# Optimization experiments

Hardware: AMD Instinct MI355X
Metric: run time of the kernel (lower is better)

Reference implementation:

```python
import jax, jax.numpy as jnp
import numpy as np

D_K, D_V, H, N = 128, 256, 256, 50
B, L = 128, 1024

def setup_inputs() -> dict:
    key = jax.random.key(0)
    ks = jax.random.split(key, 10)
    s = lambda fan_in: 1.0 / np.sqrt(fan_in)
    return {
        'problems': jax.random.normal(ks[0], (B, L, D_K), dtype=jnp.float32),
        'interactions': jax.random.normal(ks[1], (B, L, D_V), dtype=jnp.float32),
        'w_key': jax.random.uniform(ks[2], (N, D_K), jnp.float32, -s(D_K), s(D_K)),
        'w_erase_w': jax.random.uniform(ks[3], (D_V, D_V), jnp.float32, -s(D_V), s(D_V)),
        'w_erase_b': jax.random.uniform(ks[4], (D_V,), jnp.float32, -s(D_V), s(D_V)),
        'w_add_w': jax.random.uniform(ks[5], (D_V, D_V), jnp.float32, -s(D_V), s(D_V)),
        'w_add_b': jax.random.uniform(ks[6], (D_V,), jnp.float32, -s(D_V), s(D_V)),
        'w_out_w': jax.random.uniform(ks[7], (H, D_V + D_K), jnp.float32, -s(D_V + D_K), s(D_V + D_K)),
        'w_out_b': jax.random.uniform(ks[8], (H,), jnp.float32, -s(D_V + D_K), s(D_V + D_K)),
        'init_memory': jax.random.normal(ks[9], (N, D_V), dtype=jnp.float32),
    }

def reference(problems, interactions, w_key, w_erase_w, w_erase_b, w_add_w, w_add_b, w_out_w, w_out_b, init_memory):
    # Precompute per-step gates outside the scan (they do not depend on memory)
    e = jax.nn.sigmoid(jnp.einsum('bld,ed->ble', interactions, w_erase_w) + w_erase_b)  # (B,L,d_v)
    a = jnp.tanh(jnp.einsum('bld,ed->ble', interactions, w_add_w) + w_add_b)            # (B,L,d_v)
    score = jax.nn.softmax(jnp.einsum('bld,nd->bln', problems, w_key), axis=-1)          # (B,L,n)

    mem0 = jnp.broadcast_to(init_memory, (problems.shape[0], N, D_V))

    def step(memory, xs):
        sc_t, e_t, a_t = xs  # (B,n), (B,d_v), (B,d_v)
        read = jnp.einsum('bn,bnd->bd', sc_t, memory)  # weighted read
        memory = memory * (1.0 - sc_t[:, :, None] * e_t[:, None, :])
        memory = memory + sc_t[:, :, None] * a_t[:, None, :]
        return memory, read

    xs = (score.transpose(1, 0, 2), e.transpose(1, 0, 2), a.transpose(1, 0, 2))  # time-major
    _, reads = jax.lax.scan(step, mem0, xs)  # reads: (L,B,d_v)

    x = jnp.concatenate([reads.transpose(1, 0, 2), problems], axis=-1)  # (B,L,d_v+d_k)
    # dropout in eval mode = identity
    return jnp.tanh(jnp.einsum('blc,hc->blh', x, w_out_w) + w_out_b)
```

## Files before the change

### kernel.cpp

```cpp
#include <hip/hip_runtime.h>

#define B_    128
#define L_    1024
#define DK_   128
#define DV_   256
#define NS_   50
#define H_    256
#define M_    (B_ * L_)

typedef __attribute__((ext_vector_type(8))) short   short8;
typedef __attribute__((ext_vector_type(4))) float   float4v;
typedef __attribute__((ext_vector_type(4))) int     int4v;

__device__ __forceinline__ float b2f(unsigned short u) {
    unsigned int x = ((unsigned int)u) << 16;
    return __builtin_bit_cast(float, x);
}
__device__ __forceinline__ unsigned short f2b(float f) {
    unsigned int x = __builtin_bit_cast(unsigned int, f);
    x += 0x7fffu + ((x >> 16) & 1u);
    return (unsigned short)(x >> 16);
}
__device__ __forceinline__ int pack2(float lo, float hi) {
    return (int)f2b(lo) | ((int)f2b(hi) << 16);
}
__device__ __forceinline__ float sigmoid_f(float x) {
    return 1.f / (1.f + __expf(-x));
}
__device__ __forceinline__ float tanh_f(float x) {
    return 1.f - 2.f / (__expf(2.f * x) + 1.f);
}

__device__ __forceinline__ void gload_lds16(const void* g, void* l) {
    __builtin_amdgcn_global_load_lds(
        (const __attribute__((address_space(1))) void*)g,
        (__attribute__((address_space(3))) void*)l, 16, 0, 0);
}

__global__ __launch_bounds__(256) void gate_kernel(
    const float* __restrict__ X,
    const float* __restrict__ We, const float* __restrict__ be,
    const float* __restrict__ Wa, const float* __restrict__ ba,
    unsigned short* __restrict__ e_out, unsigned short* __restrict__ a_out)
{
    constexpr int K = DV_;
    const int mblk = blockIdx.x, nblk = blockIdx.y, gate = blockIdx.z;
    const float* W    = gate ? Wa : We;
    const float* bias = gate ? ba : be;
    unsigned short* out = gate ? a_out : e_out;

    __shared__ unsigned short As[128 * 40];
    __shared__ unsigned short Bs[128 * 40];

    const int tid  = threadIdx.x;
    const int lane = tid & 63, wid = tid >> 6;
    const int wm = wid >> 1, wn = wid & 1;
    const int l15 = lane & 15, quad = lane >> 4;

    float4v acc[4][4];
#pragma unroll
    for (int i = 0; i < 4; i++)
#pragma unroll
        for (int j = 0; j < 4; j++) {
            acc[i][j][0] = 0.f; acc[i][j][1] = 0.f;
            acc[i][j][2] = 0.f; acc[i][j][3] = 0.f;
        }

    const int srow = tid >> 1;
    const int scol = (tid & 1) * 16;
    const size_t Abase = ((size_t)mblk * 128 + srow) * K;
    const size_t Bbase = ((size_t)nblk * 128 + srow) * K;

    for (int k0 = 0; k0 < K; k0 += 32) {
        const float* xa = &X[Abase + k0 + scol];
        const float* xb = &W[Bbase + k0 + scol];
        float4v va0 = *(const float4v*)(xa);
        float4v va1 = *(const float4v*)(xa + 4);
        float4v va2 = *(const float4v*)(xa + 8);
        float4v va3 = *(const float4v*)(xa + 12);
        float4v vb0 = *(const float4v*)(xb);
        float4v vb1 = *(const float4v*)(xb + 4);
        float4v vb2 = *(const float4v*)(xb + 8);
        float4v vb3 = *(const float4v*)(xb + 12);
        int4v pa0, pa1, pb0, pb1;
        pa0[0] = pack2(va0[0], va0[1]); pa0[1] = pack2(va0[2], va0[3]);
        pa0[2] = pack2(va1[0], va1[1]); pa0[3] = pack2(va1[2], va1[3]);
        pa1[0] = pack2(va2[0], va2[1]); pa1[1] = pack2(va2[2], va2[3]);
        pa1[2] = pack2(va3[0], va3[1]); pa1[3] = pack2(va3[2], va3[3]);
        pb0[0] = pack2(vb0[0], vb0[1]); pb0[1] = pack2(vb0[2], vb0[3]);
        pb0[2] = pack2(vb1[0], vb1[1]); pb0[3] = pack2(vb1[2], vb1[3]);
        pb1[0] = pack2(vb2[0], vb2[1]); pb1[1] = pack2(vb2[2], vb2[3]);
        pb1[2] = pack2(vb3[0], vb3[1]); pb1[3] = pack2(vb3[2], vb3[3]);
        *(int4v*)&As[srow * 40 + scol]     = pa0;
        *(int4v*)&As[srow * 40 + scol + 8] = pa1;
        *(int4v*)&Bs[srow * 40 + scol]     = pb0;
        *(int4v*)&Bs[srow * 40 + scol + 8] = pb1;
        __syncthreads();
        short8 af[4], bf[4];
#pragma unroll
        for (int i = 0; i < 4; i++)
            af[i] = *(const short8*)&As[(64 * wm + 16 * i + l15) * 40 + quad * 8];
#pragma unroll
        for (int j = 0; j < 4; j++)
            bf[j] = *(const short8*)&Bs[(64 * wn + 16 * j + l15) * 40 + quad * 8];
#pragma unroll
        for (int i = 0; i < 4; i++)
#pragma unroll
            for (int j = 0; j < 4; j++)
                acc[i][j] = __builtin_amdgcn_mfma_f32_16x16x32_bf16(af[i], bf[j], acc[i][j], 0, 0, 0);
        __syncthreads();
    }

#pragma unroll
    for (int i = 0; i < 4; i++) {
        const int row = mblk * 128 + 64 * wm + 16 * i + quad * 4;
#pragma unroll
        for (int j = 0; j < 4; j++) {
            const int col = nblk * 128 + 64 * wn + 16 * j + l15;
            const float bv = bias[col];
#pragma unroll
            for (int r = 0; r < 4; r++) {
                float v = acc[i][j][r] + bv;
                v = gate ? tanh_f(v) : sigmoid_f(v);
                out[(size_t)(row + r) * DV_ + col] = f2b(v);
            }
        }
    }
}

__global__ __launch_bounds__(256) void score_kernel(
    const float* __restrict__ problems,
    const float* __restrict__ w_key,
    float* __restrict__ score_scan)
{
    const int rowi = blockIdx.x * 256 + threadIdx.x;
    const float* p = problems + (size_t)rowi * DK_;

    float logit[NS_];
#pragma unroll
    for (int n = 0; n < NS_; n++) logit[n] = 0.f;

    for (int k0 = 0; k0 < DK_; k0 += 4) {
        float pf0 = p[k0], pf1 = p[k0+1], pf2 = p[k0+2], pf3 = p[k0+3];
#pragma unroll
        for (int n = 0; n < NS_; n++) {
            const float* wk = &w_key[n * DK_ + k0];
            logit[n] += pf0 * wk[0] + pf1 * wk[1] + pf2 * wk[2] + pf3 * wk[3];
        }
    }

    float mx = logit[0];
#pragma unroll
    for (int n = 1; n < NS_; n++) mx = fmaxf(mx, logit[n]);
    float sum = 0.f;
#pragma unroll
    for (int n = 0; n < NS_; n++) { logit[n] = __expf(logit[n] - mx); sum += logit[n]; }
    const float inv = 1.f / sum;

    float* o = score_scan + (size_t)rowi * 64;
#pragma unroll
    for (int v = 0; v < 16; v++) {
        float4v st;
#pragma unroll
        for (int c = 0; c < 4; c++) {
            const int j = v * 4 + c;
            st[c] = (j < NS_) ? logit[j] * inv : 0.f;
        }
        *(float4v*)(o + v * 4) = st;
    }
}

#define TCH 32
#define NCH (L_ / TCH)

__global__ __launch_bounds__(256, 4) void scan_kernel(
    const float* __restrict__ score_scan,
    const unsigned short* __restrict__ e_buf,
    const unsigned short* __restrict__ a_buf,
    const float* __restrict__ init_mem,
    unsigned short* __restrict__ reads)
{
    __shared__ float          score_s[2][TCH][64];
    __shared__ unsigned short e_s[2][TCH][32];
    __shared__ unsigned short a_s[2][TCH][32];

    const int b    = blockIdx.y;
    const int dblk = blockIdx.x;
    const int tid  = threadIdx.x;
    const int w    = tid >> 6;
    const int lane = tid & 63;
    const int dsub = lane & 7;
    const int ng   = lane >> 3;
    const int dcol = w * 8 + dsub;
    const int d    = dblk * 32 + dcol;

    float M[8];
#pragma unroll
    for (int i = 0; i < 8; i++) {
        const int n = ng * 8 + i;
        M[i] = (n < NS_) ? init_mem[n * DV_ + d] : 0.f;
    }

    const size_t rb = (size_t)b * L_;

    auto stage = [&](int c, int p) {
        const int t0 = c * TCH;
#pragma unroll
        for (int i = 0; i < 2; i++) {
            const int tt = t0 + w * 8 + i * 4 + (lane >> 4);
            gload_lds16(score_scan + ((rb + tt) * 64 + (lane & 15) * 4),
                        &score_s[p][w * 8 + i * 4][0]);
        }
        if (w < 2) {
            const int tt = t0 + w * 16 + (lane >> 2);
            gload_lds16(e_buf + ((rb + tt) * DV_ + dblk * 32 + (lane & 3) * 8),
                        &e_s[p][w * 16][0]);
        } else {
            const int tt = t0 + (w - 2) * 16 + (lane >> 2);
            gload_lds16(a_buf + ((rb + tt) * DV_ + dblk * 32 + (lane & 3) * 8),
                        &a_s[p][(w - 2) * 16][0]);
        }
    };

    unsigned short* rp = reads + rb * DV_ + d;

    int p = 0;
    stage(0, 0);
    asm volatile("s_waitcnt vmcnt(0)" ::: "memory");
    __syncthreads();

    for (int c = 0; c < NCH; ++c) {
        if (c + 1 < NCH) stage(c + 1, p ^ 1);

#pragma unroll 4
        for (int tt = 0; tt < TCH; ++tt) {
            const float* sc = &score_s[p][tt][ng * 8];
            const float4v s0 = *(const float4v*)(sc);
            const float4v s1 = *(const float4v*)(sc + 4);
            const float e_cur = b2f(e_s[p][tt][dcol]);
            const float a_cur = b2f(a_s[p][tt][dcol]);

            float r = 0.f;
            const float sarr[8] = { s0[0], s0[1], s0[2], s0[3],
                                    s1[0], s1[1], s1[2], s1[3] };
#pragma unroll
            for (int i = 0; i < 8; i++) {
                const float s = sarr[i];
                r = fmaf(s, M[i], r);
                M[i] = fmaf(s, fmaf(-e_cur, M[i], a_cur), M[i]);
            }
            r += __shfl_xor(r, 8);
            r += __shfl_xor(r, 16);
            r += __shfl_xor(r, 32);
            if (ng == 0) rp[(size_t)(c * TCH + tt) * DV_] = f2b(r);
        }

        asm volatile("s_waitcnt vmcnt(0)" ::: "memory");
        __syncthreads();
        p ^= 1;
    }
}

__global__ __launch_bounds__(256) void out_kernel(
    const unsigned short* __restrict__ reads,
    const float* __restrict__ problems,
    const float* __restrict__ Wo,
    const float* __restrict__ bo,
    float* __restrict__ out)
{
    constexpr int K = DV_ + DK_;
    const int mblk = blockIdx.x, nblk = blockIdx.y;

    __shared__ unsigned short As[128 * 40];
    __shared__ unsigned short Bs[128 * 40];

    const int tid  = threadIdx.x;
    const int lane = tid & 63, wid = tid >> 6;
    const int wm = wid >> 1, wn = wid & 1;
    const int l15 = lane & 15, quad = lane >> 4;

    float4v acc[4][4];
#pragma unroll
    for (int i = 0; i < 4; i++)
#pragma unroll
        for (int j = 0; j < 4; j++) {
            acc[i][j][0] = 0.f; acc[i][j][1] = 0.f;
            acc[i][j][2] = 0.f; acc[i][j][3] = 0.f;
        }

    const int srow = tid >> 1;
    const int scol = (tid & 1) * 16;
    const size_t mrow = (size_t)mblk * 128 + srow;
    const size_t brow = (size_t)nblk * 128 + srow;

    for (int k0 = 0; k0 < K; k0 += 32) {
        const int kk = k0 + scol;
        int4v a0, a1;
        if (kk < DV_) {
            a0 = *(const int4v*)&reads[mrow * DV_ + kk];
            a1 = *(const int4v*)&reads[mrow * DV_ + kk + 8];
        } else {
            const float* pr = &problems[mrow * DK_ + (kk - DV_)];
            float4v v0 = *(const float4v*)(pr);
            float4v v1 = *(const float4v*)(pr + 4);
            float4v v2 = *(const float4v*)(pr + 8);
            float4v v3 = *(const float4v*)(pr + 12);
            a0[0] = pack2(v0[0], v0[1]); a0[1] = pack2(v0[2], v0[3]);
            a0[2] = pack2(v1[0], v1[1]); a0[3] = pack2(v1[2], v1[3]);
            a1[0] = pack2(v2[0], v2[1]); a1[1] = pack2(v2[2], v2[3]);
            a1[2] = pack2(v3[0], v3[1]); a1[3] = pack2(v3[2], v3[3]);
        }
        const float* wb = &Wo[brow * K + kk];
        float4v u0 = *(const float4v*)(wb);
        float4v u1 = *(const float4v*)(wb + 4);
        float4v u2 = *(const float4v*)(wb + 8);
        float4v u3 = *(const float4v*)(wb + 12);
        int4v b0, b1;
        b0[0] = pack2(u0[0], u0[1]); b0[1] = pack2(u0[2], u0[3]);
        b0[2] = pack2(u1[0], u1[1]); b0[3] = pack2(u1[2], u1[3]);
        b1[0] = pack2(u2[0], u2[1]); b1[1] = pack2(u2[2], u2[3]);
        b1[2] = pack2(u3[0], u3[1]); b1[3] = pack2(u3[2], u3[3]);
        *(int4v*)&As[srow * 40 + scol]     = a0;
        *(int4v*)&As[srow * 40 + scol + 8] = a1;
        *(int4v*)&Bs[srow * 40 + scol]     = b0;
        *(int4v*)&Bs[srow * 40 + scol + 8] = b1;
        __syncthreads();
        short8 af[4], bf[4];
#pragma unroll
        for (int i = 0; i < 4; i++)
            af[i] = *(const short8*)&As[(64 * wm + 16 * i + l15) * 40 + quad * 8];
#pragma unroll
        for (int j = 0; j < 4; j++)
            bf[j] = *(const short8*)&Bs[(64 * wn + 16 * j + l15) * 40 + quad * 8];
#pragma unroll
        for (int i = 0; i < 4; i++)
#pragma unroll
            for (int j = 0; j < 4; j++)
                acc[i][j] = __builtin_amdgcn_mfma_f32_16x16x32_bf16(af[i], bf[j], acc[i][j], 0, 0, 0);
        __syncthreads();
    }

#pragma unroll
    for (int i = 0; i < 4; i++) {
        const int row = mblk * 128 + 64 * wm + 16 * i + quad * 4;
#pragma unroll
        for (int j = 0; j < 4; j++) {
            const int col = nblk * 128 + 64 * wn + 16 * j + l15;
            const float bv = bo[col];
#pragma unroll
            for (int r = 0; r < 4; r++) {
                out[(size_t)(row + r) * H_ + col] = tanh_f(acc[i][j][r] + bv);
            }
        }
    }
}

extern "C" void kernel_launch(void* const* d_in, const int* in_sizes, int n_in,
                              void* d_out, int out_size, void* d_ws, size_t ws_size,
                              hipStream_t stream) {
    const float* problems  = (const float*)d_in[0];
    const float* interact  = (const float*)d_in[1];
    const float* w_key     = (const float*)d_in[2];
    const float* w_erase_w = (const float*)d_in[3];
    const float* w_erase_b = (const float*)d_in[4];
    const float* w_add_w   = (const float*)d_in[5];
    const float* w_add_b   = (const float*)d_in[6];
    const float* w_out_w   = (const float*)d_in[7];
    const float* w_out_b   = (const float*)d_in[8];
    const float* init_mem  = (const float*)d_in[9];

    char* ws = (char*)d_ws;
    const size_t SZ_BF = (size_t)M_ * DV_ * 2;
    unsigned short* e_buf = (unsigned short*)(ws);
    unsigned short* a_buf = (unsigned short*)(ws + SZ_BF);
    unsigned short* reads = (unsigned short*)(ws + 2 * SZ_BF);
    float*     score_scan = (float*)(ws + 3 * SZ_BF);

    gate_kernel<<<dim3(M_ / 128, DV_ / 128, 2), 256, 0, stream>>>(
        interact, w_erase_w, w_erase_b, w_add_w, w_add_b, e_buf, a_buf);

    score_kernel<<<M_ / 256, 256, 0, stream>>>(problems, w_key, score_scan);

    scan_kernel<<<dim3(8, B_), 256, 0, stream>>>(
        score_scan, e_buf, a_buf, init_mem, reads);

    out_kernel<<<dim3(M_ / 128, H_ / 128), 256, 0, stream>>>(
        reads, problems, w_out_w, w_out_b, (float*)d_out);
}
```

Measured before the change: 870.2 us.

## Restructure scan: 13 slots per wave, register-prefetched scores, LDS read reduction

After: 854.3 us. No clear change (-1.8%).

```diff
diff --git a/kernel.cpp b/kernel.cpp
--- a/kernel.cpp
+++ b/kernel.cpp
@@ -11,6 +11,7 @@
 typedef __attribute__((ext_vector_type(8))) short   short8;
 typedef __attribute__((ext_vector_type(4))) float   float4v;
 typedef __attribute__((ext_vector_type(4))) int     int4v;
+typedef __attribute__((ext_vector_type(2))) int     int2v;
 
 __device__ __forceinline__ float b2f(unsigned short u) {
     unsigned int x = ((unsigned int)u) << 16;
@@ -163,101 +164,139 @@
         float4v st;
 #pragma unroll
         for (int c = 0; c < 4; c++) {
-            const int j = v * 4 + c;
-            st[c] = (j < NS_) ? logit[j] * inv : 0.f;
+            const int j  = v * 4 + c;
+            const int ng = j >> 4, ii = j & 15;
+            const int n  = ng * 13 + ii;
+            st[c] = (ii < 13 && n < NS_) ? logit[n] * inv : 0.f;
         }
         *(float4v*)(o + v * 4) = st;
     }
 }
 
-#define TCH 32
+#define TCH 128
 #define NCH (L_ / TCH)
-
-__global__ __launch_bounds__(256, 4) void scan_kernel(
+#define RCH 16
+
+__global__ __launch_bounds__(256, 2) void scan_kernel(
     const float* __restrict__ score_scan,
     const unsigned short* __restrict__ e_buf,
     const unsigned short* __restrict__ a_buf,
     const float* __restrict__ init_mem,
     unsigned short* __restrict__ reads)
 {
-    __shared__ float          score_s[2][TCH][64];
-    __shared__ unsigned short e_s[2][TCH][32];
-    __shared__ unsigned short a_s[2][TCH][32];
+    __shared__ unsigned short e_s[2][TCH][64];
+    __shared__ unsigned short a_s[2][TCH][64];
+    __shared__ float          r_s[4][RCH][64];
 
     const int b    = blockIdx.y;
     const int dblk = blockIdx.x;
     const int tid  = threadIdx.x;
     const int w    = tid >> 6;
     const int lane = tid & 63;
-    const int dsub = lane & 7;
-    const int ng   = lane >> 3;
-    const int dcol = w * 8 + dsub;
-    const int d    = dblk * 32 + dcol;
-
-    float M[8];
-#pragma unroll
-    for (int i = 0; i < 8; i++) {
-        const int n = ng * 8 + i;
+    const int d    = dblk * 64 + lane;
+
+    float M[13];
+#pragma unroll
+    for (int i = 0; i < 13; i++) {
+        const int n = w * 13 + i;
         M[i] = (n < NS_) ? init_mem[n * DV_ + d] : 0.f;
     }
 
     const size_t rb = (size_t)b * L_;
+    const float* srow = score_scan + rb * 64 + w * 16;
 
     auto stage = [&](int c, int p) {
         const int t0 = c * TCH;
 #pragma unroll
-        for (int i = 0; i < 2; i++) {
-            const int tt = t0 + w * 8 + i * 4 + (lane >> 4);
-            gload_lds16(score_scan + ((rb + tt) * 64 + (lane & 15) * 4),
-                        &score_s[p][w * 8 + i * 4][0]);
-        }
-        if (w < 2) {
-            const int tt = t0 + w * 16 + (lane >> 2);
-            gload_lds16(e_buf + ((rb + tt) * DV_ + dblk * 32 + (lane & 3) * 8),
-                        &e_s[p][w * 16][0]);
-        } else {
-            const int tt = t0 + (w - 2) * 16 + (lane >> 2);
-            gload_lds16(a_buf + ((rb + tt) * DV_ + dblk * 32 + (lane & 3) * 8),
-                        &a_s[p][(w - 2) * 16][0]);
+        for (int i = 0; i < 4; i++) {
+            const int r0 = w * 32 + i * 8;
+            const int tt = t0 + r0 + (lane >> 3);
+            const size_t goff = (rb + tt) * (size_t)DV_ + dblk * 64 + (lane & 7) * 8;
+            gload_lds16(e_buf + goff, &e_s[p][r0][0]);
+            gload_lds16(a_buf + goff, &a_s[p][r0][0]);
         }
     };
 
-    unsigned short* rp = reads + rb * DV_ + d;
-
-    int p = 0;
+    float4v sc0, sc1, sc2; float sc3;
+    float4v sn0, sn1, sn2; float sn3;
+    auto loadS = [&](int t, float4v& x0, float4v& x1, float4v& x2, float& x3) {
+        const float* sp = srow + (size_t)t * 64;
+        x0 = *(const float4v*)(sp);
+        x1 = *(const float4v*)(sp + 4);
+        x2 = *(const float4v*)(sp + 8);
+        x3 = sp[12];
+    };
+
+    int pp = 0;
     stage(0, 0);
+    loadS(0, sc0, sc1, sc2, sc3);
+    loadS(1, sn0, sn1, sn2, sn3);
     asm volatile("s_waitcnt vmcnt(0)" ::: "memory");
     __syncthreads();
 
     for (int c = 0; c < NCH; ++c) {
-        if (c + 1 < NCH) stage(c + 1, p ^ 1);
-
-#pragma unroll 4
-        for (int tt = 0; tt < TCH; ++tt) {
-            const float* sc = &score_s[p][tt][ng * 8];
-            const float4v s0 = *(const float4v*)(sc);
-            const float4v s1 = *(const float4v*)(sc + 4);
-            const float e_cur = b2f(e_s[p][tt][dcol]);
-            const float a_cur = b2f(a_s[p][tt][dcol]);
-
-            float r = 0.f;
-            const float sarr[8] = { s0[0], s0[1], s0[2], s0[3],
-                                    s1[0], s1[1], s1[2], s1[3] };
-#pragma unroll
-            for (int i = 0; i < 8; i++) {
-                const float s = sarr[i];
-                r = fmaf(s, M[i], r);
-                M[i] = fmaf(s, fmaf(-e_cur, M[i], a_cur), M[i]);
+        if (c + 1 < NCH) stage(c + 1, pp ^ 1);
+
+        for (int sub = 0; sub < TCH / RCH; ++sub) {
+            const int tbase = c * TCH + sub * RCH;
+            const int lbase = sub * RCH;
+#pragma unroll
+            for (int u = 0; u < RCH; u += 2) {
+                {
+                    const float e_cur = b2f(e_s[pp][lbase + u][lane]);
+                    const float a_cur = b2f(a_s[pp][lbase + u][lane]);
+                    float r = 0.f;
+                    const float sarr[13] = { sc0[0], sc0[1], sc0[2], sc0[3],
+                                             sc1[0], sc1[1], sc1[2], sc1[3],
+                                             sc2[0], sc2[1], sc2[2], sc2[3], sc3 };
+#pragma unroll
+                    for (int i = 0; i < 13; i++) {
+                        const float s = sarr[i];
+                        r = fmaf(s, M[i], r);
+                        M[i] = fmaf(s, fmaf(-e_cur, M[i], a_cur), M[i]);
+                    }
+                    r_s[w][u][lane] = r;
+                    const int tl = tbase + u + 2;
+                    loadS(tl < L_ ? tl : L_ - 1, sc0, sc1, sc2, sc3);
+                }
+                {
+                    const float e_cur = b2f(e_s[pp][lbase + u + 1][lane]);
+                    const float a_cur = b2f(a_s[pp][lbase + u + 1][lane]);
+                    float r = 0.f;
+                    const float sarr[13] = { sn0[0], sn0[1], sn0[2], sn0[3],
+                                             sn1[0], sn1[1], sn1[2], sn1[3],
+                                             sn2[0], sn2[1], sn2[2], sn2[3], sn3 };
+#pragma unroll
+                    for (int i = 0; i < 13; i++) {
+                        const float s = sarr[i];
+                        r = fmaf(s, M[i], r);
+                        M[i] = fmaf(s, fmaf(-e_cur, M[i], a_cur), M[i]);
+                    }
+                    r_s[w][u + 1][lane] = r;
+                    const int tl = tbase + u + 3;
+                    loadS(tl < L_ ? tl : L_ - 1, sn0, sn1, sn2, sn3);
+                }
             }
-            r += __shfl_xor(r, 8);
-            r += __shfl_xor(r, 16);
-            r += __shfl_xor(r, 32);
-            if (ng == 0) rp[(size_t)(c * TCH + tt) * DV_] = f2b(r);
+            __syncthreads();
+            {
+                const int tt = tid >> 4;
+                const int d0 = (tid & 15) * 4;
+                float4v v0 = *(const float4v*)&r_s[0][tt][d0];
+                float4v v1 = *(const float4v*)&r_s[1][tt][d0];
+                float4v v2 = *(const float4v*)&r_s[2][tt][d0];
+                float4v v3 = *(const float4v*)&r_s[3][tt][d0];
+                float4v sm = (v0 + v1) + (v2 + v3);
+                int2v pk;
+                pk[0] = pack2(sm[0], sm[1]);
+                pk[1] = pack2(sm[2], sm[3]);
+                *(int2v*)&reads[(rb + tbase + tt) * (size_t)DV_ + dblk * 64 + d0] = pk;
+            }
+            __syncthreads();
         }
 
         asm volatile("s_waitcnt vmcnt(0)" ::: "memory");
         __syncthreads();
-        p ^= 1;
+        pp ^= 1;
     }
 }
 
@@ -381,7 +420,7 @@
 
     score_kernel<<<M_ / 256, 256, 0, stream>>>(problems, w_key, score_scan);
 
-    scan_kernel<<<dim3(8, B_), 256, 0, stream>>>(
+    scan_kernel<<<dim3(4, B_), 256, 0, stream>>>(
         score_scan, e_buf, a_buf, init_mem, reads);
 
     out_kernel<<<dim3(M_ / 128, H_ / 128), 256, 0, stream>>>(
```

## Remap scan so each wave owns memory slots, reduce reads via LDS

Applied to the files above, without the earlier changes.

Result: slower. 952.5 us (+9.5%).

```diff
diff --git a/kernel.cpp b/kernel.cpp
--- a/kernel.cpp
+++ b/kernel.cpp
@@ -10,6 +10,7 @@
 
 typedef __attribute__((ext_vector_type(8))) short   short8;
 typedef __attribute__((ext_vector_type(4))) float   float4v;
+typedef __attribute__((ext_vector_type(2))) float   float2v;
 typedef __attribute__((ext_vector_type(4))) int     int4v;
 
 __device__ __forceinline__ float b2f(unsigned short u) {
@@ -29,12 +30,6 @@
 }
 __device__ __forceinline__ float tanh_f(float x) {
     return 1.f - 2.f / (__expf(2.f * x) + 1.f);
-}
-
-__device__ __forceinline__ void gload_lds16(const void* g, void* l) {
-    __builtin_amdgcn_global_load_lds(
-        (const __attribute__((address_space(1))) void*)g,
-        (__attribute__((address_space(3))) void*)l, 16, 0, 0);
 }
 
 __global__ __launch_bounds__(256) void gate_kernel(
@@ -170,94 +165,93 @@
     }
 }
 
-#define TCH 32
-#define NCH (L_ / TCH)
-
-__global__ __launch_bounds__(256, 4) void scan_kernel(
+#define RCH 16
+
+__global__ __launch_bounds__(512, 4) void scan_kernel(
     const float* __restrict__ score_scan,
     const unsigned short* __restrict__ e_buf,
     const unsigned short* __restrict__ a_buf,
     const float* __restrict__ init_mem,
     unsigned short* __restrict__ reads)
 {
-    __shared__ float          score_s[2][TCH][64];
-    __shared__ unsigned short e_s[2][TCH][32];
-    __shared__ unsigned short a_s[2][TCH][32];
+    __shared__ float r_s[8][RCH][64];
 
     const int b    = blockIdx.y;
     const int dblk = blockIdx.x;
     const int tid  = threadIdx.x;
     const int w    = tid >> 6;
     const int lane = tid & 63;
-    const int dsub = lane & 7;
-    const int ng   = lane >> 3;
-    const int dcol = w * 8 + dsub;
-    const int d    = dblk * 32 + dcol;
+    const int d    = dblk * 64 + lane;
 
     float M[8];
 #pragma unroll
     for (int i = 0; i < 8; i++) {
-        const int n = ng * 8 + i;
+        const int n = w * 8 + i;
         M[i] = (n < NS_) ? init_mem[n * DV_ + d] : 0.f;
     }
 
     const size_t rb = (size_t)b * L_;
-
-    auto stage = [&](int c, int p) {
-        const int t0 = c * TCH;
-#pragma unroll
-        for (int i = 0; i < 2; i++) {
-            const int tt = t0 + w * 8 + i * 4 + (lane >> 4);
-            gload_lds16(score_scan + ((rb + tt) * 64 + (lane & 15) * 4),
-                        &score_s[p][w * 8 + i * 4][0]);
-        }
-        if (w < 2) {
-            const int tt = t0 + w * 16 + (lane >> 2);
-            gload_lds16(e_buf + ((rb + tt) * DV_ + dblk * 32 + (lane & 3) * 8),
-                        &e_s[p][w * 16][0]);
-        } else {
-            const int tt = t0 + (w - 2) * 16 + (lane >> 2);
-            gload_lds16(a_buf + ((rb + tt) * DV_ + dblk * 32 + (lane & 3) * 8),
-                        &a_s[p][(w - 2) * 16][0]);
-        }
-    };
-
-    unsigned short* rp = reads + rb * DV_ + d;
-
-    int p = 0;
-    stage(0, 0);
-    asm volatile("s_waitcnt vmcnt(0)" ::: "memory");
-    __syncthreads();
-
-    for (int c = 0; c < NCH; ++c) {
-        if (c + 1 < NCH) stage(c + 1, p ^ 1);
-
-#pragma unroll 4
-        for (int tt = 0; tt < TCH; ++tt) {
-            const float* sc = &score_s[p][tt][ng * 8];
-            const float4v s0 = *(const float4v*)(sc);
-            const float4v s1 = *(const float4v*)(sc + 4);
-            const float e_cur = b2f(e_s[p][tt][dcol]);
-            const float a_cur = b2f(a_s[p][tt][dcol]);
-
+    const float* sbase = score_scan + rb * 64 + w * 8;
+    const unsigned short* ep = e_buf + rb * DV_ + d;
+    const unsigned short* ap = a_buf + rb * DV_ + d;
+
+    float s_p[4][8];
+    unsigned short e_p[8], a_p[8];
+
+#pragma unroll
+    for (int k = 0; k < 4; k++) {
+        const float* sp = sbase + (size_t)k * 64;
+        float4v x0 = *(const float4v*)(sp);
+        float4v x1 = *(const float4v*)(sp + 4);
+        s_p[k][0] = x0[0]; s_p[k][1] = x0[1]; s_p[k][2] = x0[2]; s_p[k][3] = x0[3];
+        s_p[k][4] = x1[0]; s_p[k][5] = x1[1]; s_p[k][6] = x1[2]; s_p[k][7] = x1[3];
+    }
+#pragma unroll
+    for (int k = 0; k < 8; k++) {
+        e_p[k] = ep[(size_t)k * DV_];
+        a_p[k] = ap[(size_t)k * DV_];
+    }
+
+    for (int t0 = 0; t0 < L_; t0 += RCH) {
+#pragma unroll
+        for (int u = 0; u < RCH; u++) {
+            const float e_cur = b2f(e_p[u & 7]);
+            const float a_cur = b2f(a_p[u & 7]);
             float r = 0.f;
-            const float sarr[8] = { s0[0], s0[1], s0[2], s0[3],
-                                    s1[0], s1[1], s1[2], s1[3] };
 #pragma unroll
             for (int i = 0; i < 8; i++) {
-                const float s = sarr[i];
+                const float s = s_p[u & 3][i];
                 r = fmaf(s, M[i], r);
                 M[i] = fmaf(s, fmaf(-e_cur, M[i], a_cur), M[i]);
             }
-            r += __shfl_xor(r, 8);
-            r += __shfl_xor(r, 16);
-            r += __shfl_xor(r, 32);
-            if (ng == 0) rp[(size_t)(c * TCH + tt) * DV_] = f2b(r);
-        }
-
-        asm volatile("s_waitcnt vmcnt(0)" ::: "memory");
-        __syncthreads();
-        p ^= 1;
+            r_s[w][u][lane] = r;
+            {
+                const float* sp = sbase + (size_t)(t0 + u + 4) * 64;
+                float4v x0 = *(const float4v*)(sp);
+                float4v x1 = *(const float4v*)(sp + 4);
+                s_p[u & 3][0] = x0[0]; s_p[u & 3][1] = x0[1];
+                s_p[u & 3][2] = x0[2]; s_p[u & 3][3] = x0[3];
+                s_p[u & 3][4] = x1[0]; s_p[u & 3][5] = x1[1];
+                s_p[u & 3][6] = x1[2]; s_p[u & 3][7] = x1[3];
+            }
+            e_p[u & 7] = ep[(size_t)(t0 + u + 8) * DV_];
+            a_p[u & 7] = ap[(size_t)(t0 + u + 8) * DV_];
+        }
+
+        __syncthreads();
+        {
+            const int tt = tid >> 5;
+            const int d0 = (tid & 31) * 2;
+            float2v sm = *(const float2v*)&r_s[0][tt][d0];
+#pragma unroll
+            for (int ww = 1; ww < 8; ww++) {
+                float2v v = *(const float2v*)&r_s[ww][tt][d0];
+                sm[0] += v[0]; sm[1] += v[1];
+            }
+            *(unsigned int*)&reads[(rb + t0 + tt) * (size_t)DV_ + dblk * 64 + d0] =
+                (unsigned int)pack2(sm[0], sm[1]);
+        }
+        __syncthreads();
     }
 }
 
@@ -371,17 +365,18 @@
 
     char* ws = (char*)d_ws;
     const size_t SZ_BF = (size_t)M_ * DV_ * 2;
+    const size_t SZ_SC = (size_t)M_ * 64 * 4;
     unsigned short* e_buf = (unsigned short*)(ws);
     unsigned short* a_buf = (unsigned short*)(ws + SZ_BF);
-    unsigned short* reads = (unsigned short*)(ws + 2 * SZ_BF);
-    float*     score_scan = (float*)(ws + 3 * SZ_BF);
+    float*     score_scan = (float*)(ws + 2 * SZ_BF);
+    unsigned short* reads = (unsigned short*)(ws + 2 * SZ_BF + SZ_SC);
 
     gate_kernel<<<dim3(M_ / 128, DV_ / 128, 2), 256, 0, stream>>>(
         interact, w_erase_w, w_erase_b, w_add_w, w_add_b, e_buf, a_buf);
 
     score_kernel<<<M_ / 256, 256, 0, stream>>>(problems, w_key, score_scan);
 
-    scan_kernel<<<dim3(8, B_), 256, 0, stream>>>(
+    scan_kernel<<<dim3(4, B_), 512, 0, stream>>>(
         score_scan, e_buf, a_buf, init_mem, reads);
 
     out_kernel<<<dim3(M_ / 128, H_ / 128), 256, 0, stream>>>(
```
